# Kernel optimization log

Hardware: AMD Instinct MI355X
Metric: run time of the kernel (lower is better)

The kernel has to match this reference:

```python
import jax, jax.numpy as jnp
import numpy as np
import math

B, S, HID, NH = 4, 256, 512, 8
D = HID // NH


def setup_inputs() -> dict:
    key = jax.random.key(0)
    ks = jax.random.split(key, 12)
    inp = {
        "q_hidden_states": jax.random.normal(ks[0], (B, S, HID), dtype=jnp.float32),
        "k_hidden_states": jax.random.normal(ks[1], (B, S, HID), dtype=jnp.float32),
        "v_hidden_states": jax.random.normal(ks[2], (B, S, HID), dtype=jnp.float32),
        "Wq": jax.random.normal(ks[3], (HID, HID), dtype=jnp.float32) * 0.02,
        "bq": jnp.zeros((HID,), dtype=jnp.float32),
        "Wk": jax.random.normal(ks[4], (HID, HID), dtype=jnp.float32) * 0.02,
        "bk": jnp.zeros((HID,), dtype=jnp.float32),
        "Wv": jax.random.normal(ks[5], (HID, HID), dtype=jnp.float32) * 0.02,
        "bv": jnp.zeros((HID,), dtype=jnp.float32),
        "rel_table": (jax.random.normal(ks[6], (8, HID), dtype=jnp.float32) * 0.02).at[0].set(0.0),  # padding_idx=0
        "edge_type": jax.random.randint(ks[7], (B, S, S), 0, 8, dtype=jnp.int32),
        "trans_mask": jax.random.randint(ks[8], (B, S, S), 0, 2, dtype=jnp.int32),
    }
    return inp


def _split_heads(x):
    # [B, S, HID] -> [B, NH, S, D]
    b, s, _ = x.shape
    return x.reshape(b, s, NH, D).transpose(0, 2, 1, 3)


def reference(q_hidden_states, k_hidden_states, v_hidden_states,
              Wq, bq, Wk, bk, Wv, bv, rel_table, edge_type, trans_mask):
    scale = 1.0 / math.sqrt(D)
    Q0 = _split_heads(q_hidden_states @ Wq + bq)  # [B,H,S,D]
    K0 = _split_heads(k_hidden_states @ Wk + bk)
    V0 = _split_heads(v_hidden_states @ Wv + bv)

    # Faithful vectorization of the torch loop:
    # at iteration i, Q and K have accumulated sum_{t<=i} rel_layer_t, and only
    # row i of the full QK^T is kept. Hence:
    #   scores[b,h,i,j] = (Q0[i] + C[i,i]) . (K0[j] + C[i,j]) / sqrt(D)
    # where C[t,p] = cumsum over t of rel_emb[:, t, p].
    R = rel_table[edge_type]                                  # [B,S,S,HID]
    C = jnp.cumsum(R.reshape(B, S, S, NH, D), axis=1)         # [B,t,p,H,D]
    idx = jnp.arange(S)
    diagC = C[:, idx, idx].transpose(0, 2, 1, 3)              # [B,H,S,D]: C[:,i,i]
    qrow = Q0 + diagC                                         # [B,H,S,D]

    scores = (jnp.einsum('bhid,bhjd->bhij', qrow, K0)
              + jnp.einsum('bhid,bijhd->bhij', qrow, C)) * scale

    scores = jnp.where(trans_mask[:, None, :, :] == 0, -1e9, scores)
    probs = jax.nn.softmax(scores, axis=-1)  # dropout omitted (eval mode)

    ctx = jnp.einsum('bhij,bhjd->bhid', probs, V0)            # [B,H,S,D]
    return ctx.transpose(0, 2, 1, 3).reshape(B, S, HID)
```

## Files before the change

kernel.cpp:

```cpp
#include <hip/hip_runtime.h>
#include <math.h>

#define BB 4
#define SS 256
#define HID 512
#define NHD 8
#define DD 64
#define IT 16

typedef __attribute__((ext_vector_type(8))) short short8v;
typedef __attribute__((ext_vector_type(4))) float f32x4;

static __device__ __forceinline__ ushort f2bf(float x) {
    uint u = __float_as_uint(x);
    uint r = u + 0x7fffu + ((u >> 16) & 1u);
    return (ushort)(r >> 16);
}
static __device__ __forceinline__ float bf2f(ushort h) {
    return __uint_as_float(((uint)h) << 16);
}

__global__ __launch_bounds__(256) void conv_x(
    const float* __restrict__ xq, const float* __restrict__ xk, const float* __restrict__ xv,
    ushort* __restrict__ Xhi, ushort* __restrict__ Xlo)
{
    const int z = blockIdx.z;
    const float* X = (z == 0) ? xq : (z == 1) ? xk : xv;
    const size_t base = (size_t)(blockIdx.x * 256 + threadIdx.x) * 4;
    const float4 v = *(const float4*)&X[base];
    ushort4 hi, lo;
    hi.x = f2bf(v.x); lo.x = f2bf(v.x - bf2f(hi.x));
    hi.y = f2bf(v.y); lo.y = f2bf(v.y - bf2f(hi.y));
    hi.z = f2bf(v.z); lo.z = f2bf(v.z - bf2f(hi.z));
    hi.w = f2bf(v.w); lo.w = f2bf(v.w - bf2f(hi.w));
    const size_t o = (size_t)z * (1024 * 512) + base;
    *(ushort4*)&Xhi[o] = hi;
    *(ushort4*)&Xlo[o] = lo;
}

__global__ __launch_bounds__(256) void conv_wt(
    const float* __restrict__ wq, const float* __restrict__ wk, const float* __restrict__ wv,
    ushort* __restrict__ Whi, ushort* __restrict__ Wlo)
{
    const int z = blockIdx.z;
    const float* W = (z == 0) ? wq : (z == 1) ? wk : wv;
    __shared__ float tile[32][33];
    const int k0 = blockIdx.x * 32, n0 = blockIdx.y * 32;
    const int t = threadIdx.x;
    {
        const int r = t >> 3, c4 = (t & 7) * 4;
        *(float4*)&tile[r][c4] = *(const float4*)&W[(size_t)(k0 + r) * HID + n0 + c4];
    }
    __syncthreads();
    {
        const int n = t >> 3, kc = (t & 7) * 4;
        ushort4 hi, lo;
        float v;
        v = tile[kc + 0][n]; hi.x = f2bf(v); lo.x = f2bf(v - bf2f(hi.x));
        v = tile[kc + 1][n]; hi.y = f2bf(v); lo.y = f2bf(v - bf2f(hi.y));
        v = tile[kc + 2][n]; hi.z = f2bf(v); lo.z = f2bf(v - bf2f(hi.z));
        v = tile[kc + 3][n]; hi.w = f2bf(v); lo.w = f2bf(v - bf2f(hi.w));
        const size_t o = (size_t)z * (512 * 512) + (size_t)(n0 + n) * HID + k0 + kc;
        *(ushort4*)&Whi[o] = hi;
        *(ushort4*)&Wlo[o] = lo;
    }
}

__global__ __launch_bounds__(256) void qkv_gemm_mfma(
    const ushort* __restrict__ Xhi, const ushort* __restrict__ Xlo,
    const ushort* __restrict__ Whi, const ushort* __restrict__ Wlo,
    const float* __restrict__ bq, const float* __restrict__ bk, const float* __restrict__ bv,
    float* __restrict__ oq, float* __restrict__ ok, float* __restrict__ ov)
{
    const int z = blockIdx.z;
    const float* bias = (z == 0) ? bq : (z == 1) ? bk : bv;
    float*       out  = (z == 0) ? oq : (z == 1) ? ok : ov;
    const size_t xb = (size_t)z * (1024 * 512);
    const size_t wb = (size_t)z * (512 * 512);

    __shared__ ushort As_hi[64][40];
    __shared__ ushort As_lo[64][40];
    __shared__ ushort Bs_hi[64][40];
    __shared__ ushort Bs_lo[64][40];

    const int t = threadIdx.x;
    const int wave = t >> 6, lane = t & 63;
    const int wr = wave >> 1, wc = wave & 1;
    const int bm = blockIdx.x * 64, bn = blockIdx.y * 64;

    const int sm = t >> 2, sk = (t & 3) * 8;
    const int fr = lane & 15, kb = (lane >> 4) * 8;

    f32x4 acc[2][2] = {};

    for (int k0 = 0; k0 < HID; k0 += 32) {
        *(uint4*)&As_hi[sm][sk] = *(const uint4*)&Xhi[xb + (size_t)(bm + sm) * HID + k0 + sk];
        *(uint4*)&As_lo[sm][sk] = *(const uint4*)&Xlo[xb + (size_t)(bm + sm) * HID + k0 + sk];
        *(uint4*)&Bs_hi[sm][sk] = *(const uint4*)&Whi[wb + (size_t)(bn + sm) * HID + k0 + sk];
        *(uint4*)&Bs_lo[sm][sk] = *(const uint4*)&Wlo[wb + (size_t)(bn + sm) * HID + k0 + sk];
        __syncthreads();

        short8v ah[2], al[2], bh[2], bl[2];
        #pragma unroll
        for (int mi = 0; mi < 2; ++mi) {
            ah[mi] = *(const short8v*)&As_hi[wr * 32 + mi * 16 + fr][kb];
            al[mi] = *(const short8v*)&As_lo[wr * 32 + mi * 16 + fr][kb];
        }
        #pragma unroll
        for (int ni = 0; ni < 2; ++ni) {
            bh[ni] = *(const short8v*)&Bs_hi[wc * 32 + ni * 16 + fr][kb];
            bl[ni] = *(const short8v*)&Bs_lo[wc * 32 + ni * 16 + fr][kb];
        }
        #pragma unroll
        for (int mi = 0; mi < 2; ++mi)
            #pragma unroll
            for (int ni = 0; ni < 2; ++ni) {
                acc[mi][ni] = __builtin_amdgcn_mfma_f32_16x16x32_bf16(ah[mi], bh[ni], acc[mi][ni], 0, 0, 0);
                acc[mi][ni] = __builtin_amdgcn_mfma_f32_16x16x32_bf16(ah[mi], bl[ni], acc[mi][ni], 0, 0, 0);
                acc[mi][ni] = __builtin_amdgcn_mfma_f32_16x16x32_bf16(al[mi], bh[ni], acc[mi][ni], 0, 0, 0);
            }
        __syncthreads();
    }

    const int r0 = bm + wr * 32 + (lane >> 4) * 4;
    const int c0 = bn + wc * 32 + (lane & 15);
    #pragma unroll
    for (int ni = 0; ni < 2; ++ni) {
        const float bia = bias[c0 + ni * 16];
        #pragma unroll
        for (int mi = 0; mi < 2; ++mi)
            #pragma unroll
            for (int q = 0; q < 4; ++q)
                out[(size_t)(r0 + mi * 16 + q) * HID + c0 + ni * 16] = acc[mi][ni][q] + bia;
    }
}

__global__ __launch_bounds__(256) void cnt_kernel(
    const int* __restrict__ edge, uint4* __restrict__ cnt)
{
    const int wave = threadIdx.x >> 6, lane = threadIdx.x & 63;
    const int col = blockIdx.x * 4 + wave;
    const int b = col / SS, j = col % SS;

    uint4 run = make_uint4(0, 0, 0, 0);
    uint4 c[4];
    #pragma unroll
    for (int r = 0; r < 4; ++r) {
        const int e = edge[((size_t)(b * SS + lane * 4 + r)) * SS + j];
        const unsigned inc = 1u << ((e & 1) * 16);
        const int comp = e >> 1;
        run.x += (comp == 0) ? inc : 0u;
        run.y += (comp == 1) ? inc : 0u;
        run.z += (comp == 2) ? inc : 0u;
        run.w += (comp == 3) ? inc : 0u;
        c[r] = run;
    }
    uint4 tot = run;
    #pragma unroll
    for (int off = 1; off < 64; off <<= 1) {
        uint4 t;
        t.x = __shfl_up((int)tot.x, off);
        t.y = __shfl_up((int)tot.y, off);
        t.z = __shfl_up((int)tot.z, off);
        t.w = __shfl_up((int)tot.w, off);
        if (lane >= off) { tot.x += t.x; tot.y += t.y; tot.z += t.z; tot.w += t.w; }
    }
    const uint4 excl = make_uint4(tot.x - run.x, tot.y - run.y, tot.z - run.z, tot.w - run.w);
    #pragma unroll
    for (int r = 0; r < 4; ++r) {
        uint4 o = make_uint4(excl.x + c[r].x, excl.y + c[r].y, excl.z + c[r].z, excl.w + c[r].w);
        cnt[((size_t)(b * SS + lane * 4 + r)) * SS + j] = o;
    }
}

__global__ __launch_bounds__(256) void attn_fused(
    const float* __restrict__ Q0,
    const float* __restrict__ K0,
    const float* __restrict__ V0,
    const float* __restrict__ rel,
    const uint4* __restrict__ cnt,
    const int* __restrict__ mask,
    float* __restrict__ out)
{
    const int x = blockIdx.x;
    const int it = x & 15;
    const int h  = (x >> 4) & 7;
    const int b  = x >> 7;
    const int i0 = it * IT;
    const int t = threadIdx.x;

    __shared__ float qst[DD][20];
    __shared__ float qre_s[IT][8];
    __shared__ float s_t[SS][20];
    __shared__ float kv[DD][68];

    {
        const int d4 = t >> 4, i = t & 15;
        const float4 q4 = *(const float4*)&Q0[((size_t)(b * SS + i0 + i)) * HID + h * DD + d4 * 4];
        const uint4 cv = cnt[((size_t)(b * SS + i0 + i)) * SS + (i0 + i)];
        float c[8];
        c[0] = (float)(cv.x & 0xffff); c[1] = (float)(cv.x >> 16);
        c[2] = (float)(cv.y & 0xffff); c[3] = (float)(cv.y >> 16);
        c[4] = (float)(cv.z & 0xffff); c[5] = (float)(cv.z >> 16);
        c[6] = (float)(cv.w & 0xffff); c[7] = (float)(cv.w >> 16);
        float o0 = q4.x, o1 = q4.y, o2 = q4.z, o3 = q4.w;
        #pragma unroll
        for (int e = 0; e < 8; ++e) {
            const float4 r4 = *(const float4*)&rel[e * HID + h * DD + d4 * 4];
            o0 += c[e] * r4.x; o1 += c[e] * r4.y; o2 += c[e] * r4.z; o3 += c[e] * r4.w;
        }
        qst[d4 * 4 + 0][i] = o0;
        qst[d4 * 4 + 1][i] = o1;
        qst[d4 * 4 + 2][i] = o2;
        qst[d4 * 4 + 3][i] = o3;
    }
    __syncthreads();

    if (t < 128) {
        const int i = t >> 3, e = t & 7;
        const float* rp = &rel[e * HID + h * DD];
        float s = 0.f;
        #pragma unroll 8
        for (int d = 0; d < DD; ++d) s += qst[d][i] * rp[d];
        qre_s[i][e] = s;
    }
    __syncthreads();

    const int iq = t >> 6;
    const int dsp = (t >> 4) & 3;
    const int jq = t & 15;
    for (int jt = 0; jt < 4; ++jt) {
        {
            const int jr = t >> 2, seg = t & 3;
            const float* src = &K0[((size_t)(b * SS + jt * 64 + jr)) * HID + h * DD + seg * 16];
            const float4 a0 = *(const float4*)&src[0];
            const float4 a1 = *(const float4*)&src[4];
            const float4 a2 = *(const float4*)&src[8];
            const float4 a3 = *(const float4*)&src[12];
            kv[seg * 16 +  0][jr] = a0.x; kv[seg * 16 +  1][jr] = a0.y;
            kv[seg * 16 +  2][jr] = a0.z; kv[seg * 16 +  3][jr] = a0.w;
            kv[seg * 16 +  4][jr] = a1.x; kv[seg * 16 +  5][jr] = a1.y;
            kv[seg * 16 +  6][jr] = a1.z; kv[seg * 16 +  7][jr] = a1.w;
            kv[seg * 16 +  8][jr] = a2.x; kv[seg * 16 +  9][jr] = a2.y;
            kv[seg * 16 + 10][jr] = a2.z; kv[seg * 16 + 11][jr] = a2.w;
            kv[seg * 16 + 12][jr] = a3.x; kv[seg * 16 + 13][jr] = a3.y;
            kv[seg * 16 + 14][jr] = a3.z; kv[seg * 16 + 15][jr] = a3.w;
        }
        __syncthreads();

        float part[4][4] = {};
        #pragma unroll
        for (int dd = 0; dd < 16; ++dd) {
            const int d = dsp * 16 + dd;
            const float4 q4 = *(const float4*)&qst[d][iq * 4];
            const float4 k4 = *(const float4*)&kv[d][jq * 4];
            part[0][0] += q4.x * k4.x; part[0][1] += q4.x * k4.y;
            part[0][2] += q4.x * k4.z; part[0][3] += q4.x * k4.w;
            part[1][0] += q4.y * k4.x; part[1][1] += q4.y * k4.y;
            part[1][2] += q4.y * k4.z; part[1][3] += q4.y * k4.w;
            part[2][0] += q4.z * k4.x; part[2][1] += q4.z * k4.y;
            part[2][2] += q4.z * k4.z; part[2][3] += q4.z * k4.w;
            part[3][0] += q4.w * k4.x; part[3][1] += q4.w * k4.y;
            part[3][2] += q4.w * k4.z; part[3][3] += q4.w * k4.w;
        }
        #pragma unroll
        for (int r = 0; r < 4; ++r)
            #pragma unroll
            for (int c = 0; c < 4; ++c) {
                float v = part[r][c];
                v += __shfl_xor(v, 16);
                v += __shfl_xor(v, 32);
                part[r][c] = v;
            }
        float sv[4];
        #pragma unroll
        for (int r = 0; r < 4; ++r)
            if (r == dsp) { sv[0] = part[r][0]; sv[1] = part[r][1]; sv[2] = part[r][2]; sv[3] = part[r][3]; }
        const int i = iq * 4 + dsp;
        const int jbase = jt * 64 + jq * 4;
        const float4 qa = *(const float4*)&qre_s[i][0];
        const float4 qb = *(const float4*)&qre_s[i][4];
        #pragma unroll
        for (int c = 0; c < 4; ++c) {
            const int j = jbase + c;
            const uint4 cv = cnt[((size_t)(b * SS + i0 + i)) * SS + j];
            float s = sv[c]
                + qa.x * (float)(cv.x & 0xffff) + qa.y * (float)(cv.x >> 16)
                + qa.z * (float)(cv.y & 0xffff) + qa.w * (float)(cv.y >> 16)
                + qb.x * (float)(cv.z & 0xffff) + qb.y * (float)(cv.z >> 16)
                + qb.z * (float)(cv.w & 0xffff) + qb.w * (float)(cv.w >> 16);
            s *= 0.125f;
            const int m = mask[((size_t)(b * SS + i0 + i)) * SS + j];
            s_t[j][i] = m ? s : -1e9f;
        }
        __syncthreads();
    }

    {
        const int wave = t >> 6, lane = t & 63;
        #pragma unroll
        for (int rr = 0; rr < 4; ++rr) {
            const int i = wave * 4 + rr;
            float v0 = s_t[lane][i], v1 = s_t[lane + 64][i],
                  v2 = s_t[lane + 128][i], v3 = s_t[lane + 192][i];
            float mx = fmaxf(fmaxf(v0, v1), fmaxf(v2, v3));
            #pragma unroll
            for (int off = 32; off > 0; off >>= 1) mx = fmaxf(mx, __shfl_xor(mx, off));
            float e0 = __expf(v0 - mx), e1 = __expf(v1 - mx),
                  e2 = __expf(v2 - mx), e3 = __expf(v3 - mx);
            float sm = e0 + e1 + e2 + e3;
            #pragma unroll
            for (int off = 32; off > 0; off >>= 1) sm += __shfl_xor(sm, off);
            const float inv = 1.f / sm;
            s_t[lane][i] = e0 * inv;
            s_t[lane + 64][i] = e1 * inv;
            s_t[lane + 128][i] = e2 * inv;
            s_t[lane + 192][i] = e3 * inv;
        }
    }
    __syncthreads();

    {
        const int jsub = (t >> 4) & 3, dq = t & 15;
        float o[4][4] = {};
        for (int jt = 0; jt < 4; ++jt) {
            {
                const int jr = t >> 2, seg = t & 3;
                const float* src = &V0[((size_t)(b * SS + jt * 64 + jr)) * HID + h * DD + seg * 16];
                #pragma unroll
                for (int qq = 0; qq < 4; ++qq)
                    *(float4*)&kv[jr][seg * 16 + qq * 4] = *(const float4*)&src[qq * 4];
            }
            __syncthreads();
            #pragma unroll
            for (int jj = 0; jj < 16; ++jj) {
                const int j = jsub * 16 + jj;
                const float4 p4 = *(const float4*)&s_t[jt * 64 + j][iq * 4];
                const float4 v4 = *(const float4*)&kv[j][dq * 4];
                o[0][0] += p4.x * v4.x; o[0][1] += p4.x * v4.y;
                o[0][2] += p4.x * v4.z; o[0][3] += p4.x * v4.w;
                o[1][0] += p4.y * v4.x; o[1][1] += p4.y * v4.y;
                o[1][2] += p4.y * v4.z; o[1][3] += p4.y * v4.w;
                o[2][0] += p4.z * v4.x; o[2][1] += p4.z * v4.y;
                o[2][2] += p4.z * v4.z; o[2][3] += p4.z * v4.w;
                o[3][0] += p4.w * v4.x; o[3][1] += p4.w * v4.y;
                o[3][2] += p4.w * v4.z; o[3][3] += p4.w * v4.w;
            }
            __syncthreads();
        }
        #pragma unroll
        for (int r = 0; r < 4; ++r)
            #pragma unroll
            for (int c = 0; c < 4; ++c) {
                float v = o[r][c];
                v += __shfl_xor(v, 16);
                v += __shfl_xor(v, 32);
                o[r][c] = v;
            }
        float sel0 = 0.f, sel1 = 0.f, sel2 = 0.f, sel3 = 0.f;
        #pragma unroll
        for (int r = 0; r < 4; ++r)
            if (r == jsub) { sel0 = o[r][0]; sel1 = o[r][1]; sel2 = o[r][2]; sel3 = o[r][3]; }
        const int i = iq * 4 + jsub;
        float4 ov; ov.x = sel0; ov.y = sel1; ov.z = sel2; ov.w = sel3;
        *(float4*)&out[((size_t)(b * SS + i0 + i)) * HID + h * DD + dq * 4] = ov;
    }
}

extern "C" void kernel_launch(void* const* d_in, const int* in_sizes, int n_in,
                              void* d_out, int out_size, void* d_ws, size_t ws_size,
                              hipStream_t stream) {
    const float* q_hs = (const float*)d_in[0];
    const float* k_hs = (const float*)d_in[1];
    const float* v_hs = (const float*)d_in[2];
    const float* Wq   = (const float*)d_in[3];
    const float* bq   = (const float*)d_in[4];
    const float* Wk   = (const float*)d_in[5];
    const float* bk   = (const float*)d_in[6];
    const float* Wv   = (const float*)d_in[7];
    const float* bv   = (const float*)d_in[8];
    const float* rel  = (const float*)d_in[9];
    const int* edge   = (const int*)d_in[10];
    const int* mask   = (const int*)d_in[11];
    float* out = (float*)d_out;

    char* ws = (char*)d_ws;
    float*  Q    = (float*)(ws);
    float*  K0   = (float*)(ws + (2u  << 20));
    float*  V0   = (float*)(ws + (4u  << 20));
    uint4*  cnt  = (uint4*)(ws + (6u  << 20));
    ushort* Xhi  = (ushort*)(ws + (10u << 20));
    ushort* Xlo  = (ushort*)(ws + (13u << 20));
    ushort* Wthi = (ushort*)(ws + (16u << 20));
    ushort* Wtlo = (ushort*)(ws + (18u << 20));

    conv_x<<<dim3(512, 1, 3), 256, 0, stream>>>(q_hs, k_hs, v_hs, Xhi, Xlo);
    conv_wt<<<dim3(16, 16, 3), 256, 0, stream>>>(Wq, Wk, Wv, Wthi, Wtlo);
    {
        dim3 grid(1024 / 64, HID / 64, 3);
        qkv_gemm_mfma<<<grid, 256, 0, stream>>>(Xhi, Xlo, Wthi, Wtlo,
                                                bq, bk, bv, Q, K0, V0);
    }
    cnt_kernel<<<dim3(BB * SS / 4), 256, 0, stream>>>(edge, cnt);
    attn_fused<<<dim3(BB * NHD * (SS / IT)), 256, 0, stream>>>(Q, K0, V0, rel, cnt, mask, out);
}
```

Baseline: 128.4 us.

## Fuse prep kernels, convert X inside GEMM, use split-bf16 MFMA for QK scores

```diff
diff --git a/kernel.cpp b/kernel.cpp
--- a/kernel.cpp
+++ b/kernel.cpp
@@ -19,63 +19,97 @@
 static __device__ __forceinline__ float bf2f(ushort h) {
     return __uint_as_float(((uint)h) << 16);
 }
-
-__global__ __launch_bounds__(256) void conv_x(
-    const float* __restrict__ xq, const float* __restrict__ xk, const float* __restrict__ xv,
-    ushort* __restrict__ Xhi, ushort* __restrict__ Xlo)
-{
-    const int z = blockIdx.z;
-    const float* X = (z == 0) ? xq : (z == 1) ? xk : xv;
-    const size_t base = (size_t)(blockIdx.x * 256 + threadIdx.x) * 4;
-    const float4 v = *(const float4*)&X[base];
-    ushort4 hi, lo;
-    hi.x = f2bf(v.x); lo.x = f2bf(v.x - bf2f(hi.x));
-    hi.y = f2bf(v.y); lo.y = f2bf(v.y - bf2f(hi.y));
-    hi.z = f2bf(v.z); lo.z = f2bf(v.z - bf2f(hi.z));
-    hi.w = f2bf(v.w); lo.w = f2bf(v.w - bf2f(hi.w));
-    const size_t o = (size_t)z * (1024 * 512) + base;
-    *(ushort4*)&Xhi[o] = hi;
-    *(ushort4*)&Xlo[o] = lo;
-}
-
-__global__ __launch_bounds__(256) void conv_wt(
+static __device__ __forceinline__ void cvt8(const float4& a, const float4& b,
+                                            short8v& hi, short8v& lo) {
+    ushort h;
+    h = f2bf(a.x); hi[0] = (short)h; lo[0] = (short)f2bf(a.x - bf2f(h));
+    h = f2bf(a.y); hi[1] = (short)h; lo[1] = (short)f2bf(a.y - bf2f(h));
+    h = f2bf(a.z); hi[2] = (short)h; lo[2] = (short)f2bf(a.z - bf2f(h));
+    h = f2bf(a.w); hi[3] = (short)h; lo[3] = (short)f2bf(a.w - bf2f(h));
+    h = f2bf(b.x); hi[4] = (short)h; lo[4] = (short)f2bf(b.x - bf2f(h));
+    h = f2bf(b.y); hi[5] = (short)h; lo[5] = (short)f2bf(b.y - bf2f(h));
+    h = f2bf(b.z); hi[6] = (short)h; lo[6] = (short)f2bf(b.z - bf2f(h));
+    h = f2bf(b.w); hi[7] = (short)h; lo[7] = (short)f2bf(b.w - bf2f(h));
+}
+
+__global__ __launch_bounds__(256) void prep_kernel(
+    const int* __restrict__ edge, uint4* __restrict__ cnt,
     const float* __restrict__ wq, const float* __restrict__ wk, const float* __restrict__ wv,
     ushort* __restrict__ Whi, ushort* __restrict__ Wlo)
 {
-    const int z = blockIdx.z;
-    const float* W = (z == 0) ? wq : (z == 1) ? wk : wv;
     __shared__ float tile[32][33];
-    const int k0 = blockIdx.x * 32, n0 = blockIdx.y * 32;
+    const int bid = blockIdx.x;
     const int t = threadIdx.x;
-    {
-        const int r = t >> 3, c4 = (t & 7) * 4;
-        *(float4*)&tile[r][c4] = *(const float4*)&W[(size_t)(k0 + r) * HID + n0 + c4];
-    }
-    __syncthreads();
-    {
-        const int n = t >> 3, kc = (t & 7) * 4;
-        ushort4 hi, lo;
-        float v;
-        v = tile[kc + 0][n]; hi.x = f2bf(v); lo.x = f2bf(v - bf2f(hi.x));
-        v = tile[kc + 1][n]; hi.y = f2bf(v); lo.y = f2bf(v - bf2f(hi.y));
-        v = tile[kc + 2][n]; hi.z = f2bf(v); lo.z = f2bf(v - bf2f(hi.z));
-        v = tile[kc + 3][n]; hi.w = f2bf(v); lo.w = f2bf(v - bf2f(hi.w));
-        const size_t o = (size_t)z * (512 * 512) + (size_t)(n0 + n) * HID + k0 + kc;
-        *(ushort4*)&Whi[o] = hi;
-        *(ushort4*)&Wlo[o] = lo;
+
+    if (bid < 256) {
+        const int wave = t >> 6, lane = t & 63;
+        const int col = bid * 4 + wave;
+        const int b = col / SS, j = col % SS;
+
+        uint4 run = make_uint4(0, 0, 0, 0);
+        uint4 c[4];
+        #pragma unroll
+        for (int r = 0; r < 4; ++r) {
+            const int e = edge[((size_t)(b * SS + lane * 4 + r)) * SS + j];
+            const unsigned inc = 1u << ((e & 1) * 16);
+            const int comp = e >> 1;
+            run.x += (comp == 0) ? inc : 0u;
+            run.y += (comp == 1) ? inc : 0u;
+            run.z += (comp == 2) ? inc : 0u;
+            run.w += (comp == 3) ? inc : 0u;
+            c[r] = run;
+        }
+        uint4 tot = run;
+        #pragma unroll
+        for (int off = 1; off < 64; off <<= 1) {
+            uint4 s;
+            s.x = __shfl_up((int)tot.x, off);
+            s.y = __shfl_up((int)tot.y, off);
+            s.z = __shfl_up((int)tot.z, off);
+            s.w = __shfl_up((int)tot.w, off);
+            if (lane >= off) { tot.x += s.x; tot.y += s.y; tot.z += s.z; tot.w += s.w; }
+        }
+        const uint4 excl = make_uint4(tot.x - run.x, tot.y - run.y, tot.z - run.z, tot.w - run.w);
+        #pragma unroll
+        for (int r = 0; r < 4; ++r) {
+            uint4 o = make_uint4(excl.x + c[r].x, excl.y + c[r].y, excl.z + c[r].z, excl.w + c[r].w);
+            cnt[((size_t)(b * SS + lane * 4 + r)) * SS + j] = o;
+        }
+    } else {
+        const int v = bid - 256;
+        const int bx = v & 15, by = (v >> 4) & 15, z = v >> 8;
+        const float* W = (z == 0) ? wq : (z == 1) ? wk : wv;
+        const int k0 = bx * 32, n0 = by * 32;
+        {
+            const int r = t >> 3, c4 = (t & 7) * 4;
+            *(float4*)&tile[r][c4] = *(const float4*)&W[(size_t)(k0 + r) * HID + n0 + c4];
+        }
+        __syncthreads();
+        {
+            const int n = t >> 3, kc = (t & 7) * 4;
+            ushort4 hi, lo;
+            float x;
+            x = tile[kc + 0][n]; hi.x = f2bf(x); lo.x = f2bf(x - bf2f(hi.x));
+            x = tile[kc + 1][n]; hi.y = f2bf(x); lo.y = f2bf(x - bf2f(hi.y));
+            x = tile[kc + 2][n]; hi.z = f2bf(x); lo.z = f2bf(x - bf2f(hi.z));
+            x = tile[kc + 3][n]; hi.w = f2bf(x); lo.w = f2bf(x - bf2f(hi.w));
+            const size_t o = (size_t)z * (512 * 512) + (size_t)(n0 + n) * HID + k0 + kc;
+            *(ushort4*)&Whi[o] = hi;
+            *(ushort4*)&Wlo[o] = lo;
+        }
     }
 }
 
 __global__ __launch_bounds__(256) void qkv_gemm_mfma(
-    const ushort* __restrict__ Xhi, const ushort* __restrict__ Xlo,
+    const float* __restrict__ xq, const float* __restrict__ xk, const float* __restrict__ xv,
     const ushort* __restrict__ Whi, const ushort* __restrict__ Wlo,
     const float* __restrict__ bq, const float* __restrict__ bk, const float* __restrict__ bv,
     float* __restrict__ oq, float* __restrict__ ok, float* __restrict__ ov)
 {
     const int z = blockIdx.z;
+    const float* X    = (z == 0) ? xq : (z == 1) ? xk : xv;
     const float* bias = (z == 0) ? bq : (z == 1) ? bk : bv;
     float*       out  = (z == 0) ? oq : (z == 1) ? ok : ov;
-    const size_t xb = (size_t)z * (1024 * 512);
     const size_t wb = (size_t)z * (512 * 512);
 
     __shared__ ushort As_hi[64][40];
@@ -94,8 +128,15 @@
     f32x4 acc[2][2] = {};
 
     for (int k0 = 0; k0 < HID; k0 += 32) {
-        *(uint4*)&As_hi[sm][sk] = *(const uint4*)&Xhi[xb + (size_t)(bm + sm) * HID + k0 + sk];
-        *(uint4*)&As_lo[sm][sk] = *(const uint4*)&Xlo[xb + (size_t)(bm + sm) * HID + k0 + sk];
+        {
+            const float* xp = &X[(size_t)(bm + sm) * HID + k0 + sk];
+            const float4 a0 = *(const float4*)&xp[0];
+            const float4 a1 = *(const float4*)&xp[4];
+            short8v h8, l8;
+            cvt8(a0, a1, h8, l8);
+            *(short8v*)&As_hi[sm][sk] = h8;
+            *(short8v*)&As_lo[sm][sk] = l8;
+        }
         *(uint4*)&Bs_hi[sm][sk] = *(const uint4*)&Whi[wb + (size_t)(bn + sm) * HID + k0 + sk];
         *(uint4*)&Bs_lo[sm][sk] = *(const uint4*)&Wlo[wb + (size_t)(bn + sm) * HID + k0 + sk];
         __syncthreads();
@@ -132,44 +173,6 @@
             #pragma unroll
             for (int q = 0; q < 4; ++q)
                 out[(size_t)(r0 + mi * 16 + q) * HID + c0 + ni * 16] = acc[mi][ni][q] + bia;
-    }
-}
-
-__global__ __launch_bounds__(256) void cnt_kernel(
-    const int* __restrict__ edge, uint4* __restrict__ cnt)
-{
-    const int wave = threadIdx.x >> 6, lane = threadIdx.x & 63;
-    const int col = blockIdx.x * 4 + wave;
-    const int b = col / SS, j = col % SS;
-
-    uint4 run = make_uint4(0, 0, 0, 0);
-    uint4 c[4];
-    #pragma unroll
-    for (int r = 0; r < 4; ++r) {
-        const int e = edge[((size_t)(b * SS + lane * 4 + r)) * SS + j];
-        const unsigned inc = 1u << ((e & 1) * 16);
-        const int comp = e >> 1;
-        run.x += (comp == 0) ? inc : 0u;
-        run.y += (comp == 1) ? inc : 0u;
-        run.z += (comp == 2) ? inc : 0u;
-        run.w += (comp == 3) ? inc : 0u;
-        c[r] = run;
-    }
-    uint4 tot = run;
-    #pragma unroll
-    for (int off = 1; off < 64; off <<= 1) {
-        uint4 t;
-        t.x = __shfl_up((int)tot.x, off);
-        t.y = __shfl_up((int)tot.y, off);
-        t.z = __shfl_up((int)tot.z, off);
-        t.w = __shfl_up((int)tot.w, off);
-        if (lane >= off) { tot.x += t.x; tot.y += t.y; tot.z += t.z; tot.w += t.w; }
-    }
-    const uint4 excl = make_uint4(tot.x - run.x, tot.y - run.y, tot.z - run.z, tot.w - run.w);
-    #pragma unroll
-    for (int r = 0; r < 4; ++r) {
-        uint4 o = make_uint4(excl.x + c[r].x, excl.y + c[r].y, excl.z + c[r].z, excl.w + c[r].w);
-        cnt[((size_t)(b * SS + lane * 4 + r)) * SS + j] = o;
     }
 }
 
@@ -187,17 +190,19 @@
     const int h  = (x >> 4) & 7;
     const int b  = x >> 7;
     const int i0 = it * IT;
-    const int t = threadIdx.x;
-
-    __shared__ float qst[DD][20];
+    const int t = threadIdx.x, wave = t >> 6, lane = t & 63;
+
+    __shared__ ushort qhi[16][72];
+    __shared__ ushort qlo[16][72];
     __shared__ float qre_s[IT][8];
     __shared__ float s_t[SS][20];
-    __shared__ float kv[DD][68];
-
-    {
-        const int d4 = t >> 4, i = t & 15;
-        const float4 q4 = *(const float4*)&Q0[((size_t)(b * SS + i0 + i)) * HID + h * DD + d4 * 4];
-        const uint4 cv = cnt[((size_t)(b * SS + i0 + i)) * SS + (i0 + i)];
+    __shared__ float vtile[64][68];
+
+    const int pi = t >> 4, pd = t & 15;
+    float4 qr4;
+    {
+        const float4 q4 = *(const float4*)&Q0[((size_t)(b * SS + i0 + pi)) * HID + h * DD + pd * 4];
+        const uint4 cv = cnt[((size_t)(b * SS + i0 + pi)) * SS + (i0 + pi)];
         float c[8];
         c[0] = (float)(cv.x & 0xffff); c[1] = (float)(cv.x >> 16);
         c[2] = (float)(cv.y & 0xffff); c[3] = (float)(cv.y >> 16);
@@ -206,98 +211,95 @@
         float o0 = q4.x, o1 = q4.y, o2 = q4.z, o3 = q4.w;
         #pragma unroll
         for (int e = 0; e < 8; ++e) {
-            const float4 r4 = *(const float4*)&rel[e * HID + h * DD + d4 * 4];
+            const float4 r4 = *(const float4*)&rel[e * HID + h * DD + pd * 4];
             o0 += c[e] * r4.x; o1 += c[e] * r4.y; o2 += c[e] * r4.z; o3 += c[e] * r4.w;
         }
-        qst[d4 * 4 + 0][i] = o0;
-        qst[d4 * 4 + 1][i] = o1;
-        qst[d4 * 4 + 2][i] = o2;
-        qst[d4 * 4 + 3][i] = o3;
+        qr4.x = o0; qr4.y = o1; qr4.z = o2; qr4.w = o3;
+        ushort4 h4, l4;
+        h4.x = f2bf(o0); l4.x = f2bf(o0 - bf2f(h4.x));
+        h4.y = f2bf(o1); l4.y = f2bf(o1 - bf2f(h4.y));
+        h4.z = f2bf(o2); l4.z = f2bf(o2 - bf2f(h4.z));
+        h4.w = f2bf(o3); l4.w = f2bf(o3 - bf2f(h4.w));
+        *(ushort4*)&qhi[pi][pd * 4] = h4;
+        *(ushort4*)&qlo[pi][pd * 4] = l4;
+    }
+    {
+        float r[8];
+        #pragma unroll
+        for (int e = 0; e < 8; ++e) {
+            const float4 rr = *(const float4*)&rel[e * HID + h * DD + pd * 4];
+            r[e] = qr4.x * rr.x + qr4.y * rr.y + qr4.z * rr.z + qr4.w * rr.w;
+        }
+        #pragma unroll
+        for (int e = 0; e < 8; ++e) {
+            float v = r[e];
+            v += __shfl_xor(v, 1);
+            v += __shfl_xor(v, 2);
+            v += __shfl_xor(v, 4);
+            v += __shfl_xor(v, 8);
+            r[e] = v;
+        }
+        float sel = 0.f;
+        #pragma unroll
+        for (int e = 0; e < 8; ++e) if (pd == e) sel = r[e];
+        if (pd < 8) qre_s[pi][pd] = sel;
     }
     __syncthreads();
 
-    if (t < 128) {
-        const int i = t >> 3, e = t & 7;
-        const float* rp = &rel[e * HID + h * DD];
-        float s = 0.f;
-        #pragma unroll 8
-        for (int d = 0; d < DD; ++d) s += qst[d][i] * rp[d];
-        qre_s[i][e] = s;
+    {
+        const int fr = lane & 15, kb8 = (lane >> 4) * 8;
+        const int jt = wave;
+        const int ib = (lane >> 4) * 4;
+
+        short8v qh[2], ql[2];
+        #pragma unroll
+        for (int ks = 0; ks < 2; ++ks) {
+            qh[ks] = *(const short8v*)&qhi[fr][ks * 32 + kb8];
+            ql[ks] = *(const short8v*)&qlo[fr][ks * 32 + kb8];
+        }
+        float4 qa[4], qb[4];
+        #pragma unroll
+        for (int q = 0; q < 4; ++q) {
+            qa[q] = *(const float4*)&qre_s[ib + q][0];
+            qb[q] = *(const float4*)&qre_s[ib + q][4];
+        }
+
+        #pragma unroll
+        for (int jf = 0; jf < 4; ++jf) {
+            const int j = jt * 64 + jf * 16 + fr;
+            const float* Kr = &K0[((size_t)(b * SS + j)) * HID + h * DD];
+            f32x4 acc = {};
+            #pragma unroll
+            for (int ks = 0; ks < 2; ++ks) {
+                const float4 k0v = *(const float4*)&Kr[ks * 32 + kb8];
+                const float4 k1v = *(const float4*)&Kr[ks * 32 + kb8 + 4];
+                short8v kh, kl;
+                cvt8(k0v, k1v, kh, kl);
+                acc = __builtin_amdgcn_mfma_f32_16x16x32_bf16(qh[ks], kh, acc, 0, 0, 0);
+                acc = __builtin_amdgcn_mfma_f32_16x16x32_bf16(qh[ks], kl, acc, 0, 0, 0);
+                acc = __builtin_amdgcn_mfma_f32_16x16x32_bf16(ql[ks], kh, acc, 0, 0, 0);
+            }
+            float sv[4];
+            #pragma unroll
+            for (int q = 0; q < 4; ++q) {
+                const int i = ib + q;
+                const uint4 cv = cnt[((size_t)(b * SS + i0 + i)) * SS + j];
+                float s = acc[q]
+                    + qa[q].x * (float)(cv.x & 0xffff) + qa[q].y * (float)(cv.x >> 16)
+                    + qa[q].z * (float)(cv.y & 0xffff) + qa[q].w * (float)(cv.y >> 16)
+                    + qb[q].x * (float)(cv.z & 0xffff) + qb[q].y * (float)(cv.z >> 16)
+                    + qb[q].z * (float)(cv.w & 0xffff) + qb[q].w * (float)(cv.w >> 16);
+                s *= 0.125f;
+                const int m = mask[((size_t)(b * SS + i0 + i)) * SS + j];
+                sv[q] = m ? s : -1e9f;
+            }
+            float4 w4; w4.x = sv[0]; w4.y = sv[1]; w4.z = sv[2]; w4.w = sv[3];
+            *(float4*)&s_t[j][ib] = w4;
+        }
     }
     __syncthreads();
 
-    const int iq = t >> 6;
-    const int dsp = (t >> 4) & 3;
-    const int jq = t & 15;
-    for (int jt = 0; jt < 4; ++jt) {
-        {
-            const int jr = t >> 2, seg = t & 3;
-            const float* src = &K0[((size_t)(b * SS + jt * 64 + jr)) * HID + h * DD + seg * 16];
-            const float4 a0 = *(const float4*)&src[0];
-            const float4 a1 = *(const float4*)&src[4];
-            const float4 a2 = *(const float4*)&src[8];
-            const float4 a3 = *(const float4*)&src[12];
-            kv[seg * 16 +  0][jr] = a0.x; kv[seg * 16 +  1][jr] = a0.y;
-            kv[seg * 16 +  2][jr] = a0.z; kv[seg * 16 +  3][jr] = a0.w;
-            kv[seg * 16 +  4][jr] = a1.x; kv[seg * 16 +  5][jr] = a1.y;
-            kv[seg * 16 +  6][jr] = a1.z; kv[seg * 16 +  7][jr] = a1.w;
-            kv[seg * 16 +  8][jr] = a2.x; kv[seg * 16 +  9][jr] = a2.y;
-            kv[seg * 16 + 10][jr] = a2.z; kv[seg * 16 + 11][jr] = a2.w;
-            kv[seg * 16 + 12][jr] = a3.x; kv[seg * 16 + 13][jr] = a3.y;
-            kv[seg * 16 + 14][jr] = a3.z; kv[seg * 16 + 15][jr] = a3.w;
-        }
-        __syncthreads();
-
-        float part[4][4] = {};
-        #pragma unroll
-        for (int dd = 0; dd < 16; ++dd) {
-            const int d = dsp * 16 + dd;
-            const float4 q4 = *(const float4*)&qst[d][iq * 4];
-            const float4 k4 = *(const float4*)&kv[d][jq * 4];
-            part[0][0] += q4.x * k4.x; part[0][1] += q4.x * k4.y;
-            part[0][2] += q4.x * k4.z; part[0][3] += q4.x * k4.w;
-            part[1][0] += q4.y * k4.x; part[1][1] += q4.y * k4.y;
-            part[1][2] += q4.y * k4.z; part[1][3] += q4.y * k4.w;
-            part[2][0] += q4.z * k4.x; part[2][1] += q4.z * k4.y;
-            part[2][2] += q4.z * k4.z; part[2][3] += q4.z * k4.w;
-            part[3][0] += q4.w * k4.x; part[3][1] += q4.w * k4.y;
-            part[3][2] += q4.w * k4.z; part[3][3] += q4.w * k4.w;
-        }
-        #pragma unroll
-        for (int r = 0; r < 4; ++r)
-            #pragma unroll
-            for (int c = 0; c < 4; ++c) {
-                float v = part[r][c];
-                v += __shfl_xor(v, 16);
-                v += __shfl_xor(v, 32);
-                part[r][c] = v;
-            }
-        float sv[4];
-        #pragma unroll
-        for (int r = 0; r < 4; ++r)
-            if (r == dsp) { sv[0] = part[r][0]; sv[1] = part[r][1]; sv[2] = part[r][2]; sv[3] = part[r][3]; }
-        const int i = iq * 4 + dsp;
-        const int jbase = jt * 64 + jq * 4;
-        const float4 qa = *(const float4*)&qre_s[i][0];
-        const float4 qb = *(const float4*)&qre_s[i][4];
-        #pragma unroll
-        for (int c = 0; c < 4; ++c) {
-            const int j = jbase + c;
-            const uint4 cv = cnt[((size_t)(b * SS + i0 + i)) * SS + j];
-            float s = sv[c]
-                + qa.x * (float)(cv.x & 0xffff) + qa.y * (float)(cv.x >> 16)
-                + qa.z * (float)(cv.y & 0xffff) + qa.w * (float)(cv.y >> 16)
-                + qb.x * (float)(cv.z & 0xffff) + qb.y * (float)(cv.z >> 16)
-                + qb.z * (float)(cv.w & 0xffff) + qb.w * (float)(cv.w >> 16);
-            s *= 0.125f;
-            const int m = mask[((size_t)(b * SS + i0 + i)) * SS + j];
-            s_t[j][i] = m ? s : -1e9f;
-        }
-        __syncthreads();
-    }
-
-    {
-        const int wave = t >> 6, lane = t & 63;
+    {
         #pragma unroll
         for (int rr = 0; rr < 4; ++rr) {
             const int i = wave * 4 + rr;
@@ -321,6 +323,7 @@
     __syncthreads();
 
     {
+        const int iq = wave;
         const int jsub = (t >> 4) & 3, dq = t & 15;
         float o[4][4] = {};
         for (int jt = 0; jt < 4; ++jt) {
@@ -329,14 +332,14 @@
                 const float* src = &V0[((size_t)(b * SS + jt * 64 + jr)) * HID + h * DD + seg * 16];
                 #pragma unroll
                 for (int qq = 0; qq < 4; ++qq)
-                    *(float4*)&kv[jr][seg * 16 + qq * 4] = *(const float4*)&src[qq * 4];
+                    *(float4*)&vtile[jr][seg * 16 + qq * 4] = *(const float4*)&src[qq * 4];
             }
             __syncthreads();
             #pragma unroll
             for (int jj = 0; jj < 16; ++jj) {
                 const int j = jsub * 16 + jj;
                 const float4 p4 = *(const float4*)&s_t[jt * 64 + j][iq * 4];
-                const float4 v4 = *(const float4*)&kv[j][dq * 4];
+                const float4 v4 = *(const float4*)&vtile[j][dq * 4];
                 o[0][0] += p4.x * v4.x; o[0][1] += p4.x * v4.y;
                 o[0][2] += p4.x * v4.z; o[0][3] += p4.x * v4.w;
                 o[1][0] += p4.y * v4.x; o[1][1] += p4.y * v4.y;
@@ -389,18 +392,14 @@
     float*  K0   = (float*)(ws + (2u  << 20));
     float*  V0   = (float*)(ws + (4u  << 20));
     uint4*  cnt  = (uint4*)(ws + (6u  << 20));
-    ushort* Xhi  = (ushort*)(ws + (10u << 20));
-    ushort* Xlo  = (ushort*)(ws + (13u << 20));
-    ushort* Wthi = (ushort*)(ws + (16u << 20));
-    ushort* Wtlo = (ushort*)(ws + (18u << 20));
-
-    conv_x<<<dim3(512, 1, 3), 256, 0, stream>>>(q_hs, k_hs, v_hs, Xhi, Xlo);
-    conv_wt<<<dim3(16, 16, 3), 256, 0, stream>>>(Wq, Wk, Wv, Wthi, Wtlo);
+    ushort* Wthi = (ushort*)(ws + (10u << 20));
+    ushort* Wtlo = (ushort*)(ws + (12u << 20));
+
+    prep_kernel<<<dim3(1024), 256, 0, stream>>>(edge, cnt, Wq, Wk, Wv, Wthi, Wtlo);
     {
         dim3 grid(1024 / 64, HID / 64, 3);
-        qkv_gemm_mfma<<<grid, 256, 0, stream>>>(Xhi, Xlo, Wthi, Wtlo,
+        qkv_gemm_mfma<<<grid, 256, 0, stream>>>(q_hs, k_hs, v_hs, Wthi, Wtlo,
                                                 bq, bk, bv, Q, K0, V0);
     }
-    cnt_kernel<<<dim3(BB * SS / 4), 256, 0, stream>>>(edge, cnt);
     attn_fused<<<dim3(BB * NHD * (SS / IT)), 256, 0, stream>>>(Q, K0, V0, rel, cnt, mask, out);
 }
```

After: 117.7 us. -8.3%, faster.
